# Performance work log

Measured on AMD Instinct MI355X. Metric: run time of the kernel, lower is better.

Reference implementation:

```python
import jax, jax.numpy as jnp
import numpy as np

EMBED_DIM = 512
NUM_HEADS = 8
HEAD_DIM = EMBED_DIM // NUM_HEADS


def setup_inputs() -> dict:
    key = jax.random.key(0)
    k1, k2, kw, kb, kow, kob = jax.random.split(key, 6)
    B, L, C = 2, 2048, EMBED_DIM
    s = 1.0 / np.sqrt(C)
    return {
        "x1": jax.random.normal(k1, (B, L, C), dtype=jnp.float32),
        "x2": jax.random.normal(k2, (B, L, C), dtype=jnp.float32),
        # nn.Linear(embed_dim, 3*embed_dim): weight [3C, C], bias [3C]
        "qkv_w": jax.random.uniform(kw, (3 * C, C), jnp.float32, -s, s),
        "qkv_b": jax.random.uniform(kb, (3 * C,), jnp.float32, -s, s),
        # nn.Linear(embed_dim, embed_dim): weight [C, C], bias [C]
        "out_w": jax.random.uniform(kow, (C, C), jnp.float32, -s, s),
        "out_b": jax.random.uniform(kob, (C,), jnp.float32, -s, s),
    }


def _qkv(x, qkv_w, qkv_b):
    B, L, C = x.shape
    H, D = NUM_HEADS, C // NUM_HEADS
    # Linear: x @ W^T + b, then view(B, L, H, 3, D) and split along the '3' axis
    qkv = (jnp.einsum("blc,fc->blf", x, qkv_w) + qkv_b).reshape(B, L, H, 3, D)
    qkv = jnp.transpose(qkv, (3, 0, 2, 1, 4))  # [3, B, H, L, D]
    return qkv[0], qkv[1], qkv[2]


def _attend(q, k, v):
    # q,k,v: [B, H, L, D]; scale by 1/sqrt(D)
    scale = 1.0 / np.sqrt(q.shape[-1]).astype(np.float32)
    scores = jnp.einsum("bhqd,bhkd->bhqk", q, k) * scale  # [B,H,L,L]
    attn = jax.nn.softmax(scores, axis=-1)
    out = jnp.einsum("bhqk,bhkd->bhqd", attn, v)
    B, H, L, D = out.shape
    return jnp.transpose(out, (0, 2, 1, 3)).reshape(B, L, H * D)


def reference(x1, x2, qkv_w, qkv_b, out_w, out_b):
    q1, k1, v1 = _qkv(x1, qkv_w, qkv_b)
    q2, k2, v2 = _qkv(x2, qkv_w, qkv_b)
    out1 = _attend(q1, k2, v2)  # q from x1, k/v from x2
    out2 = _attend(q2, k1, v1)  # q from x2, k/v from x1
    out1 = jnp.einsum("blc,fc->blf", out1, out_w) + out_b
    out2 = jnp.einsum("blc,fc->blf", out2, out_w) + out_b
    return (out1, out2)
```

## Files before the change

### kernel.cpp

```cpp
#include <hip/hip_runtime.h>
#include <stdint.h>

typedef unsigned short u16;
typedef unsigned int u32;
typedef short bf16x8 __attribute__((ext_vector_type(8)));
typedef float f32x4 __attribute__((ext_vector_type(4)));

#define K_DIM 512

__device__ __forceinline__ u16 f2bf(float f) {
  union { float f; u32 u; } v; v.f = f;
  return (u16)((v.u + 0x8000u) >> 16);
}
__device__ __forceinline__ u32 pk2(float lo, float hi) {
  union { float f; u32 u; } a, b; a.f = lo; b.f = hi;
  return __builtin_amdgcn_perm(b.u + 0x8000u, a.u + 0x8000u, 0x07060302u);
}

__global__ void cvt_kernel(const float* __restrict__ x1, const float* __restrict__ x2,
                           const float* __restrict__ qkvw, const float* __restrict__ outw,
                           u16* __restrict__ xb, u16* __restrict__ wqkv, u16* __restrict__ wout) {
  int tid = blockIdx.x * 256 + threadIdx.x;
  const float4* src; u16* dst; int idx = tid;
  if (idx < 524288)        { src = (const float4*)x1;   dst = xb; }
  else if (idx < 1048576)  { src = (const float4*)x2;   dst = xb + 2097152; idx -= 524288; }
  else if (idx < 1245184)  { src = (const float4*)qkvw; dst = wqkv;         idx -= 1048576; }
  else                     { src = (const float4*)outw; dst = wout;         idx -= 1245184; }
  float4 v = src[idx];
  *(uint2*)&dst[idx * 4] = make_uint2(pk2(v.x, v.y), pk2(v.z, v.w));
}

#define LDA 40

__global__ __launch_bounds__(256, 3) void qkv_gemm(
    const u16* __restrict__ A, const u16* __restrict__ W, const float* __restrict__ bias,
    u16* __restrict__ qb, u16* __restrict__ kb, u16* __restrict__ vtb) {
  __shared__ __align__(16) u16 As[2][128 * LDA];
  __shared__ __align__(16) u16 Bs[2][128 * LDA];
  const int t = threadIdx.x;
  const int m0 = blockIdx.x * 128, n0 = blockIdx.y * 128;
  const int lane = t & 63, l16 = lane & 15, quad = lane >> 4;
  const int w = t >> 6;
  const int wm = (w >> 1) * 64, wn = (w & 1) * 64;
  const int sr = t >> 2, sc = (t & 3) * 8;

  const u16* Ap = A + (size_t)(m0 + sr) * K_DIM + sc;
  const u16* Wp = W + (size_t)(n0 + sr) * K_DIM + sc;

  f32x4 acc[4][4];
#pragma unroll
  for (int i = 0; i < 4; ++i)
#pragma unroll
    for (int j = 0; j < 4; ++j) acc[i][j] = (f32x4){0.f, 0.f, 0.f, 0.f};

  uint4 ra0 = *(const uint4*)(Ap);
  uint4 ra1 = *(const uint4*)(Ap + 64 * K_DIM);
  uint4 rb0 = *(const uint4*)(Wp);
  uint4 rb1 = *(const uint4*)(Wp + 64 * K_DIM);
  *(uint4*)&As[0][sr * LDA + sc] = ra0;
  *(uint4*)&As[0][(sr + 64) * LDA + sc] = ra1;
  *(uint4*)&Bs[0][sr * LDA + sc] = rb0;
  *(uint4*)&Bs[0][(sr + 64) * LDA + sc] = rb1;
  ra0 = *(const uint4*)(Ap + 32);
  ra1 = *(const uint4*)(Ap + 64 * K_DIM + 32);
  rb0 = *(const uint4*)(Wp + 32);
  rb1 = *(const uint4*)(Wp + 64 * K_DIM + 32);
  __syncthreads();

  for (int kt = 0; kt < 16; ++kt) {
    const int cur = kt & 1, nxt = cur ^ 1;
    if (kt < 15) {
      *(uint4*)&As[nxt][sr * LDA + sc] = ra0;
      *(uint4*)&As[nxt][(sr + 64) * LDA + sc] = ra1;
      *(uint4*)&Bs[nxt][sr * LDA + sc] = rb0;
      *(uint4*)&Bs[nxt][(sr + 64) * LDA + sc] = rb1;
    }
    if (kt < 14) {
      int ko = (kt + 2) * 32;
      ra0 = *(const uint4*)(Ap + ko);
      ra1 = *(const uint4*)(Ap + 64 * K_DIM + ko);
      rb0 = *(const uint4*)(Wp + ko);
      rb1 = *(const uint4*)(Wp + 64 * K_DIM + ko);
    }
    bf16x8 af[4], bfr[4];
#pragma unroll
    for (int mi = 0; mi < 4; ++mi)
      af[mi] = *(const bf16x8*)&As[cur][(wm + mi * 16 + l16) * LDA + quad * 8];
#pragma unroll
    for (int ni = 0; ni < 4; ++ni)
      bfr[ni] = *(const bf16x8*)&Bs[cur][(wn + ni * 16 + l16) * LDA + quad * 8];
#pragma unroll
    for (int mi = 0; mi < 4; ++mi)
#pragma unroll
      for (int ni = 0; ni < 4; ++ni)
        acc[mi][ni] = __builtin_amdgcn_mfma_f32_16x16x32_bf16(bfr[ni], af[mi], acc[mi][ni], 0, 0, 0);
    __syncthreads();
  }

  const int fbase = n0 + wn;
  const int h = fbase / 192;
  const int s = (fbase - h * 192) >> 6;
  float4 bv[4];
#pragma unroll
  for (int ni = 0; ni < 4; ++ni)
    bv[ni] = *(const float4*)&bias[fbase + ni * 16 + quad * 4];
  const int bh = m0 >> 11;
  const int lbase = (m0 & 2047) + wm;

  if (s == 2) {
    u16* dst = vtb + (size_t)((bh * 8 + h) * 64) * 2048;
#pragma unroll
    for (int mi = 0; mi < 4; ++mi) {
      int l = lbase + mi * 16 + l16;
#pragma unroll
      for (int ni = 0; ni < 4; ++ni)
#pragma unroll
        for (int r = 0; r < 4; ++r)
          dst[(ni * 16 + quad * 4 + r) * 2048 + l] = f2bf(acc[mi][ni][r] + bv[ni][r]);
    }
  } else {
    u16* dst = (s == 0 ? qb : kb) + (size_t)((bh * 8 + h) * 2048) * 64;
    const float sc2 = (s == 0) ? 0.18033688011112042f : 1.0f;
#pragma unroll
    for (int mi = 0; mi < 4; ++mi) {
      int l = lbase + mi * 16 + l16;
#pragma unroll
      for (int ni = 0; ni < 4; ++ni) {
        float v0 = (acc[mi][ni][0] + bv[ni][0]) * sc2;
        float v1 = (acc[mi][ni][1] + bv[ni][1]) * sc2;
        float v2 = (acc[mi][ni][2] + bv[ni][2]) * sc2;
        float v3 = (acc[mi][ni][3] + bv[ni][3]) * sc2;
        *(uint2*)&dst[(size_t)l * 64 + ni * 16 + quad * 4] = make_uint2(pk2(v0, v1), pk2(v2, v3));
      }
    }
  }
}

#define LQ 72
#define LP 80

__global__ __launch_bounds__(256, 2) void attn_kernel(
    const u16* __restrict__ qb, const u16* __restrict__ kb, const u16* __restrict__ vtb,
    u16* __restrict__ attnb) {
  __shared__ __align__(16) u16 Ks[2][64 * LQ];
  __shared__ __align__(16) u16 VTs[2][64 * LQ];
  __shared__ __align__(16) u16 Ps[128 * LP];

  const int t = threadIdx.x;
  const int w = t >> 6, lane = t & 63, l16 = lane & 15, quad = lane >> 4;
  const int bid = blockIdx.x;
  const int qt = bid & 15;
  const int comb = bid >> 4;
  const int h = comb & 7, bb = (comb >> 3) & 1, pair = comb >> 4;
  const int in_q = pair, in_kv = pair ^ 1;

  const u16* Qg = qb + (size_t)((in_q * 2 + bb) * 8 + h) * 2048 * 64;
  const u16* Kg = kb + (size_t)((in_kv * 2 + bb) * 8 + h) * 2048 * 64;
  const u16* Vg = vtb + (size_t)((in_kv * 2 + bb) * 8 + h) * 64 * 2048;

#pragma unroll
  for (int u = 0; u < 4; ++u) {
    int idx = u * 256 + t;
    int row = idx >> 3, seg = (idx & 7) * 8;
    *(uint4*)&Ps[row * LP + seg] = *(const uint4*)(Qg + (qt * 128 + row) * 64 + seg);
  }

  const int srow = t >> 3, sseg = (t & 7) * 8;
  uint4 rk0 = *(const uint4*)(Kg + srow * 64 + sseg);
  uint4 rk1 = *(const uint4*)(Kg + (srow + 32) * 64 + sseg);
  uint4 rv0 = *(const uint4*)(Vg + srow * 2048 + sseg);
  uint4 rv1 = *(const uint4*)(Vg + (srow + 32) * 2048 + sseg);
  *(uint4*)&Ks[0][srow * LQ + sseg] = rk0;
  *(uint4*)&Ks[0][(srow + 32) * LQ + sseg] = rk1;
  *(uint4*)&VTs[0][srow * LQ + sseg] = rv0;
  *(uint4*)&VTs[0][(srow + 32) * LQ + sseg] = rv1;
  rk0 = *(const uint4*)(Kg + (64 + srow) * 64 + sseg);
  rk1 = *(const uint4*)(Kg + (64 + srow + 32) * 64 + sseg);
  rv0 = *(const uint4*)(Vg + srow * 2048 + 64 + sseg);
  rv1 = *(const uint4*)(Vg + (srow + 32) * 2048 + 64 + sseg);
  __syncthreads();

  bf16x8 qf[2][2];
#pragma unroll
  for (int mi = 0; mi < 2; ++mi)
#pragma unroll
    for (int ks = 0; ks < 2; ++ks)
      qf[mi][ks] = *(const bf16x8*)&Ps[(w * 32 + mi * 16 + l16) * LP + ks * 32 + quad * 8];

  f32x4 oacc[2][4];
  float rs[2] = {0.f, 0.f};
#pragma unroll
  for (int mi = 0; mi < 2; ++mi)
#pragma unroll
    for (int ni = 0; ni < 4; ++ni) oacc[mi][ni] = (f32x4){0.f, 0.f, 0.f, 0.f};

  u16* Pw = &Ps[w * 32 * LP];

  for (int kt = 0; kt < 32; ++kt) {
    const int cur = kt & 1, nxt = cur ^ 1;
    if (kt < 31) {
      *(uint4*)&Ks[nxt][srow * LQ + sseg] = rk0;
      *(uint4*)&Ks[nxt][(srow + 32) * LQ + sseg] = rk1;
      *(uint4*)&VTs[nxt][srow * LQ + sseg] = rv0;
      *(uint4*)&VTs[nxt][(srow + 32) * LQ + sseg] = rv1;
    }
    if (kt < 30) {
      int ko = (kt + 2) * 64;
      rk0 = *(const uint4*)(Kg + (ko + srow) * 64 + sseg);
      rk1 = *(const uint4*)(Kg + (ko + srow + 32) * 64 + sseg);
      rv0 = *(const uint4*)(Vg + srow * 2048 + ko + sseg);
      rv1 = *(const uint4*)(Vg + (srow + 32) * 2048 + ko + sseg);
    }

    f32x4 sacc[2][4];
#pragma unroll
    for (int mi = 0; mi < 2; ++mi)
#pragma unroll
      for (int ni = 0; ni < 4; ++ni) sacc[mi][ni] = (f32x4){0.f, 0.f, 0.f, 0.f};
#pragma unroll
    for (int ks = 0; ks < 2; ++ks) {
      bf16x8 kfr[4];
#pragma unroll
      for (int ni = 0; ni < 4; ++ni)
        kfr[ni] = *(const bf16x8*)&Ks[cur][(ni * 16 + l16) * LQ + ks * 32 + quad * 8];
#pragma unroll
      for (int mi = 0; mi < 2; ++mi)
#pragma unroll
        for (int ni = 0; ni < 4; ++ni)
          sacc[mi][ni] = __builtin_amdgcn_mfma_f32_16x16x32_bf16(kfr[ni], qf[mi][ks], sacc[mi][ni], 0, 0, 0);
    }

#pragma unroll
    for (int mi = 0; mi < 2; ++mi)
#pragma unroll
      for (int ni = 0; ni < 4; ++ni) {
        float p0 = exp2f(sacc[mi][ni][0]);
        float p1 = exp2f(sacc[mi][ni][1]);
        float p2 = exp2f(sacc[mi][ni][2]);
        float p3 = exp2f(sacc[mi][ni][3]);
        rs[mi] += (p0 + p1) + (p2 + p3);
        *(uint2*)&Pw[(mi * 16 + l16) * LP + ni * 16 + quad * 4] = make_uint2(pk2(p0, p1), pk2(p2, p3));
      }

#pragma unroll
    for (int ks = 0; ks < 2; ++ks) {
      bf16x8 vf[4], pf[2];
#pragma unroll
      for (int ni = 0; ni < 4; ++ni)
        vf[ni] = *(const bf16x8*)&VTs[cur][(ni * 16 + l16) * LQ + ks * 32 + quad * 8];
#pragma unroll
      for (int mi = 0; mi < 2; ++mi)
        pf[mi] = *(const bf16x8*)&Pw[(mi * 16 + l16) * LP + ks * 32 + quad * 8];
#pragma unroll
      for (int mi = 0; mi < 2; ++mi)
#pragma unroll
        for (int ni = 0; ni < 4; ++ni)
          oacc[mi][ni] = __builtin_amdgcn_mfma_f32_16x16x32_bf16(vf[ni], pf[mi], oacc[mi][ni], 0, 0, 0);
    }
    __syncthreads();
  }

  float inv[2];
#pragma unroll
  for (int mi = 0; mi < 2; ++mi) {
    float s = rs[mi];
    s += __shfl_xor(s, 16);
    s += __shfl_xor(s, 32);
    inv[mi] = 1.0f / s;
  }
  const int mbase = in_q * 4096 + bb * 2048 + qt * 128 + w * 32;
#pragma unroll
  for (int mi = 0; mi < 2; ++mi) {
    int row = mbase + mi * 16 + l16;
#pragma unroll
    for (int ni = 0; ni < 4; ++ni) {
      float v0 = oacc[mi][ni][0] * inv[mi];
      float v1 = oacc[mi][ni][1] * inv[mi];
      float v2 = oacc[mi][ni][2] * inv[mi];
      float v3 = oacc[mi][ni][3] * inv[mi];
      *(uint2*)&attnb[(size_t)row * 512 + h * 64 + ni * 16 + quad * 4] =
          make_uint2(pk2(v0, v1), pk2(v2, v3));
    }
  }
}

__global__ __launch_bounds__(256, 2) void out_gemm(
    const u16* __restrict__ A, const u16* __restrict__ W, const float* __restrict__ bias,
    float* __restrict__ out) {
  __shared__ __align__(16) u16 As[2][64 * LDA];
  __shared__ __align__(16) u16 Bs[2][128 * LDA];
  const int t = threadIdx.x;
  const int m0 = blockIdx.x * 64, n0 = blockIdx.y * 128;
  const int lane = t & 63, l16 = lane & 15, quad = lane >> 4;
  const int w = t >> 6;
  const int wm = (w & 1) * 32, wn = (w >> 1) * 64;
  const int ar = t >> 2, ac = (t & 3) * 8;
  const int sr = t >> 2, sc = (t & 3) * 8;

  const u16* Ap = A + (size_t)(m0 + ar) * K_DIM + ac;
  const u16* Wp = W + (size_t)(n0 + sr) * K_DIM + sc;

  f32x4 acc[2][4];
#pragma unroll
  for (int i = 0; i < 2; ++i)
#pragma unroll
    for (int j = 0; j < 4; ++j) acc[i][j] = (f32x4){0.f, 0.f, 0.f, 0.f};

  uint4 ra = *(const uint4*)Ap;
  uint4 rb0 = *(const uint4*)(Wp);
  uint4 rb1 = *(const uint4*)(Wp + 64 * K_DIM);
  *(uint4*)&As[0][ar * LDA + ac] = ra;
  *(uint4*)&Bs[0][sr * LDA + sc] = rb0;
  *(uint4*)&Bs[0][(sr + 64) * LDA + sc] = rb1;
  ra = *(const uint4*)(Ap + 32);
  rb0 = *(const uint4*)(Wp + 32);
  rb1 = *(const uint4*)(Wp + 64 * K_DIM + 32);
  __syncthreads();

  for (int kt = 0; kt < 16; ++kt) {
    const int cur = kt & 1, nxt = cur ^ 1;
    if (kt < 15) {
      *(uint4*)&As[nxt][ar * LDA + ac] = ra;
      *(uint4*)&Bs[nxt][sr * LDA + sc] = rb0;
      *(uint4*)&Bs[nxt][(sr + 64) * LDA + sc] = rb1;
    }
    if (kt < 14) {
      int ko = (kt + 2) * 32;
      ra = *(const uint4*)(Ap + ko);
      rb0 = *(const uint4*)(Wp + ko);
      rb1 = *(const uint4*)(Wp + 64 * K_DIM + ko);
    }
    bf16x8 af[2], bfr[4];
#pragma unroll
    for (int mi = 0; mi < 2; ++mi)
      af[mi] = *(const bf16x8*)&As[cur][(wm + mi * 16 + l16) * LDA + quad * 8];
#pragma unroll
    for (int ni = 0; ni < 4; ++ni)
      bfr[ni] = *(const bf16x8*)&Bs[cur][(wn + ni * 16 + l16) * LDA + quad * 8];
#pragma unroll
    for (int mi = 0; mi < 2; ++mi)
#pragma unroll
      for (int ni = 0; ni < 4; ++ni)
        acc[mi][ni] = __builtin_amdgcn_mfma_f32_16x16x32_bf16(af[mi], bfr[ni], acc[mi][ni], 0, 0, 0);
    __syncthreads();
  }

#pragma unroll
  for (int ni = 0; ni < 4; ++ni) {
    int f = n0 + wn + ni * 16 + l16;
    float bv = bias[f];
#pragma unroll
    for (int mi = 0; mi < 2; ++mi)
#pragma unroll
      for (int r = 0; r < 4; ++r) {
        int m = m0 + wm + mi * 16 + quad * 4 + r;
        out[(size_t)m * 512 + f] = acc[mi][ni][r] + bv;
      }
  }
}

extern "C" void kernel_launch(void* const* d_in, const int* in_sizes, int n_in,
                              void* d_out, int out_size, void* d_ws, size_t ws_size,
                              hipStream_t stream) {
  const float* x1   = (const float*)d_in[0];
  const float* x2   = (const float*)d_in[1];
  const float* qkvw = (const float*)d_in[2];
  const float* qkvb = (const float*)d_in[3];
  const float* outw = (const float*)d_in[4];
  const float* outb = (const float*)d_in[5];
  float* out = (float*)d_out;
  char* ws = (char*)d_ws;

  u16* xb    = (u16*)(ws + 0);
  u16* wqkv  = (u16*)(ws + 8388608);
  u16* wout  = (u16*)(ws + 9961472);
  u16* qb    = (u16*)(ws + 10485760);
  u16* kb    = (u16*)(ws + 18874368);
  u16* vtb   = (u16*)(ws + 27262976);
  u16* attnb = (u16*)(ws + 0);

  cvt_kernel<<<5120, 256, 0, stream>>>(x1, x2, qkvw, outw, xb, wqkv, wout);

  dim3 g1(64, 12);
  qkv_gemm<<<g1, 256, 0, stream>>>(xb, wqkv, qkvb, qb, kb, vtb);

  attn_kernel<<<512, 256, 0, stream>>>(qb, kb, vtb, attnb);

  dim3 g3(128, 4);
  out_gemm<<<g3, 256, 0, stream>>>(attnb, wout, outb, out);
}
```

Measured before the change: 175.5 us.

## Use 512-thread attention blocks with 16 query rows per warp, single-buffered K/V

The attention kernel now launches 512 threads per block, with eight waves each owning 16 query rows instead of four waves owning 32. The K/V shared tiles drop from double to single buffering, with a register prefetch one tile ahead and an extra barrier per tile. exp2f is replaced by the hardware exp2 builtin and the P tile padding shrinks. The aim is higher occupancy and latency hiding through more waves, at the cost of less per-wave K/V fragment reuse, more barriers and less prefetch distance.

Result: faster. 164.4 us (-6.4%).

```diff
diff --git a/kernel.cpp b/kernel.cpp
--- a/kernel.cpp
+++ b/kernel.cpp
@@ -137,13 +137,13 @@
 }
 
 #define LQ 72
-#define LP 80
-
-__global__ __launch_bounds__(256, 2) void attn_kernel(
+#define LP 72
+
+__global__ __launch_bounds__(512, 4) void attn_kernel(
     const u16* __restrict__ qb, const u16* __restrict__ kb, const u16* __restrict__ vtb,
     u16* __restrict__ attnb) {
-  __shared__ __align__(16) u16 Ks[2][64 * LQ];
-  __shared__ __align__(16) u16 VTs[2][64 * LQ];
+  __shared__ __align__(16) u16 Ks[64 * LQ];
+  __shared__ __align__(16) u16 VTs[64 * LQ];
   __shared__ __align__(16) u16 Ps[128 * LP];
 
   const int t = threadIdx.x;
@@ -159,128 +159,89 @@
   const u16* Vg = vtb + (size_t)((in_kv * 2 + bb) * 8 + h) * 64 * 2048;
 
 #pragma unroll
-  for (int u = 0; u < 4; ++u) {
-    int idx = u * 256 + t;
+  for (int u = 0; u < 2; ++u) {
+    int idx = u * 512 + t;
     int row = idx >> 3, seg = (idx & 7) * 8;
     *(uint4*)&Ps[row * LP + seg] = *(const uint4*)(Qg + (qt * 128 + row) * 64 + seg);
   }
-
   const int srow = t >> 3, sseg = (t & 7) * 8;
-  uint4 rk0 = *(const uint4*)(Kg + srow * 64 + sseg);
-  uint4 rk1 = *(const uint4*)(Kg + (srow + 32) * 64 + sseg);
-  uint4 rv0 = *(const uint4*)(Vg + srow * 2048 + sseg);
-  uint4 rv1 = *(const uint4*)(Vg + (srow + 32) * 2048 + sseg);
-  *(uint4*)&Ks[0][srow * LQ + sseg] = rk0;
-  *(uint4*)&Ks[0][(srow + 32) * LQ + sseg] = rk1;
-  *(uint4*)&VTs[0][srow * LQ + sseg] = rv0;
-  *(uint4*)&VTs[0][(srow + 32) * LQ + sseg] = rv1;
-  rk0 = *(const uint4*)(Kg + (64 + srow) * 64 + sseg);
-  rk1 = *(const uint4*)(Kg + (64 + srow + 32) * 64 + sseg);
-  rv0 = *(const uint4*)(Vg + srow * 2048 + 64 + sseg);
-  rv1 = *(const uint4*)(Vg + (srow + 32) * 2048 + 64 + sseg);
+  uint4 rk = *(const uint4*)(Kg + srow * 64 + sseg);
+  uint4 rv = *(const uint4*)(Vg + srow * 2048 + sseg);
   __syncthreads();
 
-  bf16x8 qf[2][2];
-#pragma unroll
-  for (int mi = 0; mi < 2; ++mi)
-#pragma unroll
-    for (int ks = 0; ks < 2; ++ks)
-      qf[mi][ks] = *(const bf16x8*)&Ps[(w * 32 + mi * 16 + l16) * LP + ks * 32 + quad * 8];
-
-  f32x4 oacc[2][4];
-  float rs[2] = {0.f, 0.f};
-#pragma unroll
-  for (int mi = 0; mi < 2; ++mi)
-#pragma unroll
-    for (int ni = 0; ni < 4; ++ni) oacc[mi][ni] = (f32x4){0.f, 0.f, 0.f, 0.f};
-
-  u16* Pw = &Ps[w * 32 * LP];
+  bf16x8 qf[2];
+#pragma unroll
+  for (int ks = 0; ks < 2; ++ks)
+    qf[ks] = *(const bf16x8*)&Ps[(w * 16 + l16) * LP + ks * 32 + quad * 8];
+
+  f32x4 oacc[4];
+  float rs = 0.f;
+#pragma unroll
+  for (int ni = 0; ni < 4; ++ni) oacc[ni] = (f32x4){0.f, 0.f, 0.f, 0.f};
+
+  u16* Pw = &Ps[w * 16 * LP];
 
   for (int kt = 0; kt < 32; ++kt) {
-    const int cur = kt & 1, nxt = cur ^ 1;
+    *(uint4*)&Ks[srow * LQ + sseg] = rk;
+    *(uint4*)&VTs[srow * LQ + sseg] = rv;
+    __syncthreads();
     if (kt < 31) {
-      *(uint4*)&Ks[nxt][srow * LQ + sseg] = rk0;
-      *(uint4*)&Ks[nxt][(srow + 32) * LQ + sseg] = rk1;
-      *(uint4*)&VTs[nxt][srow * LQ + sseg] = rv0;
-      *(uint4*)&VTs[nxt][(srow + 32) * LQ + sseg] = rv1;
-    }
-    if (kt < 30) {
-      int ko = (kt + 2) * 64;
-      rk0 = *(const uint4*)(Kg + (ko + srow) * 64 + sseg);
-      rk1 = *(const uint4*)(Kg + (ko + srow + 32) * 64 + sseg);
-      rv0 = *(const uint4*)(Vg + srow * 2048 + ko + sseg);
-      rv1 = *(const uint4*)(Vg + (srow + 32) * 2048 + ko + sseg);
-    }
-
-    f32x4 sacc[2][4];
-#pragma unroll
-    for (int mi = 0; mi < 2; ++mi)
-#pragma unroll
-      for (int ni = 0; ni < 4; ++ni) sacc[mi][ni] = (f32x4){0.f, 0.f, 0.f, 0.f};
+      int ko = (kt + 1) * 64;
+      rk = *(const uint4*)(Kg + (ko + srow) * 64 + sseg);
+      rv = *(const uint4*)(Vg + srow * 2048 + ko + sseg);
+    }
+
+    f32x4 sacc[4];
+#pragma unroll
+    for (int ni = 0; ni < 4; ++ni) sacc[ni] = (f32x4){0.f, 0.f, 0.f, 0.f};
 #pragma unroll
     for (int ks = 0; ks < 2; ++ks) {
       bf16x8 kfr[4];
 #pragma unroll
       for (int ni = 0; ni < 4; ++ni)
-        kfr[ni] = *(const bf16x8*)&Ks[cur][(ni * 16 + l16) * LQ + ks * 32 + quad * 8];
-#pragma unroll
-      for (int mi = 0; mi < 2; ++mi)
-#pragma unroll
-        for (int ni = 0; ni < 4; ++ni)
-          sacc[mi][ni] = __builtin_amdgcn_mfma_f32_16x16x32_bf16(kfr[ni], qf[mi][ks], sacc[mi][ni], 0, 0, 0);
-    }
-
-#pragma unroll
-    for (int mi = 0; mi < 2; ++mi)
-#pragma unroll
-      for (int ni = 0; ni < 4; ++ni) {
-        float p0 = exp2f(sacc[mi][ni][0]);
-        float p1 = exp2f(sacc[mi][ni][1]);
-        float p2 = exp2f(sacc[mi][ni][2]);
-        float p3 = exp2f(sacc[mi][ni][3]);
-        rs[mi] += (p0 + p1) + (p2 + p3);
-        *(uint2*)&Pw[(mi * 16 + l16) * LP + ni * 16 + quad * 4] = make_uint2(pk2(p0, p1), pk2(p2, p3));
-      }
+        kfr[ni] = *(const bf16x8*)&Ks[(ni * 16 + l16) * LQ + ks * 32 + quad * 8];
+#pragma unroll
+      for (int ni = 0; ni < 4; ++ni)
+        sacc[ni] = __builtin_amdgcn_mfma_f32_16x16x32_bf16(kfr[ni], qf[ks], sacc[ni], 0, 0, 0);
+    }
+
+#pragma unroll
+    for (int ni = 0; ni < 4; ++ni) {
+      float p0 = __builtin_amdgcn_exp2f(sacc[ni][0]);
+      float p1 = __builtin_amdgcn_exp2f(sacc[ni][1]);
+      float p2 = __builtin_amdgcn_exp2f(sacc[ni][2]);
+      float p3 = __builtin_amdgcn_exp2f(sacc[ni][3]);
+      rs += (p0 + p1) + (p2 + p3);
+      *(uint2*)&Pw[l16 * LP + ni * 16 + quad * 4] = make_uint2(pk2(p0, p1), pk2(p2, p3));
+    }
 
 #pragma unroll
     for (int ks = 0; ks < 2; ++ks) {
-      bf16x8 vf[4], pf[2];
-#pragma unroll
-      for (int ni = 0; ni < 4; ++ni)
-        vf[ni] = *(const bf16x8*)&VTs[cur][(ni * 16 + l16) * LQ + ks * 32 + quad * 8];
-#pragma unroll
-      for (int mi = 0; mi < 2; ++mi)
-        pf[mi] = *(const bf16x8*)&Pw[(mi * 16 + l16) * LP + ks * 32 + quad * 8];
-#pragma unroll
-      for (int mi = 0; mi < 2; ++mi)
-#pragma unroll
-        for (int ni = 0; ni < 4; ++ni)
-          oacc[mi][ni] = __builtin_amdgcn_mfma_f32_16x16x32_bf16(vf[ni], pf[mi], oacc[mi][ni], 0, 0, 0);
+      bf16x8 vf[4];
+#pragma unroll
+      for (int ni = 0; ni < 4; ++ni)
+        vf[ni] = *(const bf16x8*)&VTs[(ni * 16 + l16) * LQ + ks * 32 + quad * 8];
+      bf16x8 pf = *(const bf16x8*)&Pw[l16 * LP + ks * 32 + quad * 8];
+#pragma unroll
+      for (int ni = 0; ni < 4; ++ni)
+        oacc[ni] = __builtin_amdgcn_mfma_f32_16x16x32_bf16(vf[ni], pf, oacc[ni], 0, 0, 0);
     }
     __syncthreads();
   }
 
-  float inv[2];
-#pragma unroll
-  for (int mi = 0; mi < 2; ++mi) {
-    float s = rs[mi];
-    s += __shfl_xor(s, 16);
-    s += __shfl_xor(s, 32);
-    inv[mi] = 1.0f / s;
-  }
-  const int mbase = in_q * 4096 + bb * 2048 + qt * 128 + w * 32;
-#pragma unroll
-  for (int mi = 0; mi < 2; ++mi) {
-    int row = mbase + mi * 16 + l16;
-#pragma unroll
-    for (int ni = 0; ni < 4; ++ni) {
-      float v0 = oacc[mi][ni][0] * inv[mi];
-      float v1 = oacc[mi][ni][1] * inv[mi];
-      float v2 = oacc[mi][ni][2] * inv[mi];
-      float v3 = oacc[mi][ni][3] * inv[mi];
-      *(uint2*)&attnb[(size_t)row * 512 + h * 64 + ni * 16 + quad * 4] =
-          make_uint2(pk2(v0, v1), pk2(v2, v3));
-    }
+  float s = rs;
+  s += __shfl_xor(s, 16);
+  s += __shfl_xor(s, 32);
+  const float inv = 1.0f / s;
+  const int row = in_q * 4096 + bb * 2048 + qt * 128 + w * 16 + l16;
+#pragma unroll
+  for (int ni = 0; ni < 4; ++ni) {
+    float v0 = oacc[ni][0] * inv;
+    float v1 = oacc[ni][1] * inv;
+    float v2 = oacc[ni][2] * inv;
+    float v3 = oacc[ni][3] * inv;
+    *(uint2*)&attnb[(size_t)row * 512 + h * 64 + ni * 16 + quad * 4] =
+        make_uint2(pk2(v0, v1), pk2(v2, v3));
   }
 }
 
@@ -384,7 +345,7 @@
   dim3 g1(64, 12);
   qkv_gemm<<<g1, 256, 0, stream>>>(xb, wqkv, qkvb, qb, kb, vtb);
 
-  attn_kernel<<<512, 256, 0, stream>>>(qb, kb, vtb, attnb);
+  attn_kernel<<<512, 512, 0, stream>>>(qb, kb, vtb, attnb);
 
   dim3 g3(128, 4);
   out_gemm<<<g3, 256, 0, stream>>>(attnb, wout, outb, out);
```
